# Performance work log

Hardware: AMD Instinct MI355X
Metric: run time of the kernel (lower is better)

Reference implementation:

```python
import jax, jax.numpy as jnp
import numpy as np
import math

B, S, H, DH = 8, 1024, 12, 64
HID = H * DH  # 768


def setup_inputs() -> dict:
    key = jax.random.key(0)
    ks = jax.random.split(key, 6)
    hidden_states = jax.random.normal(ks[0], (B, S, HID), dtype=jnp.float32)
    attention_mask = jax.random.bernoulli(ks[1], 0.1, (B, 1, 1, S))
    rel_pos = jax.random.normal(ks[2], (B, H, S, S), dtype=jnp.float32) * 0.1
    rel_2d_pos = jax.random.normal(ks[3], (B, H, S, S), dtype=jnp.float32) * 0.1
    W_qkv = jax.random.normal(ks[4], (HID, 3 * HID), dtype=jnp.float32) * (1.0 / math.sqrt(HID))
    q_bias = jnp.zeros((1, 1, HID), dtype=jnp.float32)
    v_bias = jnp.zeros((1, 1, HID), dtype=jnp.float32)
    return {
        "hidden_states": hidden_states,
        "attention_mask": attention_mask,
        "rel_pos": rel_pos,
        "rel_2d_pos": rel_2d_pos,
        "W_qkv": W_qkv,
        "q_bias": q_bias,
        "v_bias": v_bias,
    }


def reference(hidden_states, attention_mask, rel_pos, rel_2d_pos, W_qkv, q_bias, v_bias):
    b, s, _ = hidden_states.shape
    # fast_qkv: single GEMM, no bias; q/v get learned additive biases
    qkv = hidden_states @ W_qkv                       # [B,S,3*HID]
    q, k, v = jnp.split(qkv, 3, axis=-1)
    q = q + q_bias
    v = v + v_bias
    # [B,S,HID] -> [B,H,S,DH]
    def to_heads(x):
        return x.reshape(b, s, H, DH).transpose(0, 2, 1, 3)
    q, k, v = to_heads(q), to_heads(k), to_heads(v)
    q = q / math.sqrt(DH)
    scores = jnp.einsum('bhqd,bhkd->bhqk', q, k)      # [B,H,S,S]
    scores = scores + rel_pos + rel_2d_pos
    scores = jnp.where(attention_mask, -jnp.inf, scores.astype(jnp.float32))
    probs = jax.nn.softmax(scores, axis=-1).astype(v.dtype)
    context = jnp.einsum('bhqk,bhkd->bhqd', probs, v)  # [B,H,S,DH]
    context = context.transpose(0, 2, 1, 3).reshape(b, s, HID)
    return (context, probs)
```

## Files before the change

kernel.cpp:

```cpp
#include <hip/hip_runtime.h>
#include <hip/hip_bf16.h>

typedef __attribute__((ext_vector_type(8))) short short8;
typedef __attribute__((ext_vector_type(4))) float f32x4;

#define NB 8
#define NS 1024
#define NH 12
#define ND 64
#define NHID 768
#define N3 2304

#define SBAR() __builtin_amdgcn_sched_barrier(0)

__device__ __forceinline__ unsigned short f2bf(float f) {
  __hip_bfloat16 h = __float2bfloat16(f);
  return *reinterpret_cast<unsigned short*>(&h);
}
__device__ __forceinline__ float bf2f(unsigned short u) {
  __hip_bfloat16 h;
  *reinterpret_cast<unsigned short*>(&h) = u;
  return __bfloat162float(h);
}

__device__ __forceinline__ void gload_lds16(const unsigned short* g, unsigned short* l) {
  __builtin_amdgcn_global_load_lds(
      (const __attribute__((address_space(1))) unsigned int*)g,
      (__attribute__((address_space(3))) unsigned int*)l, 16, 0, 0);
}

__global__ void k_cast(const float* __restrict__ in, unsigned short* __restrict__ out, int n4) {
  int i = blockIdx.x * blockDim.x + threadIdx.x;
  if (i >= n4) return;
  float4 v = ((const float4*)in)[i];
  ushort4 o;
  o.x = f2bf(v.x); o.y = f2bf(v.y); o.z = f2bf(v.z); o.w = f2bf(v.w);
  ((ushort4*)out)[i] = o;
}

__global__ void k_mask(const int* __restrict__ mask, unsigned long long* __restrict__ bits) {
  int b = blockIdx.x, t = threadIdx.x;
  unsigned long long bal = __ballot(mask[b * NS + t] != 0);
  if ((t & 63) == 0) bits[b * 16 + (t >> 6)] = bal;
}

__global__ __launch_bounds__(256) void k_wt(const float* __restrict__ W, unsigned short* __restrict__ Wt) {
  __shared__ float tile[32][33];
  int r0 = blockIdx.x * 32;
  int c0 = blockIdx.y * 32;
  int tx = threadIdx.x & 31, ty = threadIdx.x >> 5;
#pragma unroll
  for (int p = 0; p < 4; ++p)
    tile[ty + 8*p][tx] = W[(size_t)(r0 + ty + 8*p) * N3 + c0 + tx];
  __syncthreads();
#pragma unroll
  for (int p = 0; p < 4; ++p)
    Wt[(size_t)(c0 + ty + 8*p) * NHID + r0 + tx] = f2bf(tile[tx][ty + 8*p]);
}

__global__ __launch_bounds__(256) void k_qkv(const unsigned short* __restrict__ A,
                                             const unsigned short* __restrict__ Wt,
                                             const float* __restrict__ qb,
                                             const float* __restrict__ vb,
                                             unsigned short* __restrict__ out) {
  __shared__ __align__(16) unsigned short As[128 * 32];
  __shared__ __align__(16) unsigned short Bs[128 * 32];
  const int t = threadIdx.x;
  const int w = t >> 6, l = t & 63, l15 = l & 15, lhi = l >> 4;
  const int wr = w >> 1, wc = w & 1;
  const int rowbase = blockIdx.x * 128;
  const int colbase = blockIdx.y * 128;
  const int srow = l >> 2;
  const int scol = (l & 3) * 8;

  f32x4 acc[4][4] = {};

  for (int k0 = 0; k0 < NHID; k0 += 32) {
    __syncthreads();
#pragma unroll
    for (int i = 0; i < 2; ++i) {
      int rr = w * 32 + i * 16;
      gload_lds16(A  + (size_t)(rowbase + rr + srow) * NHID + k0 + scol, As + rr * 32);
      gload_lds16(Wt + (size_t)(colbase + rr + srow) * NHID + k0 + scol, Bs + rr * 32);
    }
    __syncthreads();
    short8 a[4], bfr[4];
#pragma unroll
    for (int mi = 0; mi < 4; ++mi)
      a[mi] = *(const short8*)(As + (wr * 64 + mi * 16 + l15) * 32 + lhi * 8);
#pragma unroll
    for (int ni = 0; ni < 4; ++ni)
      bfr[ni] = *(const short8*)(Bs + (wc * 64 + ni * 16 + l15) * 32 + lhi * 8);
#pragma unroll
    for (int mi = 0; mi < 4; ++mi)
#pragma unroll
      for (int ni = 0; ni < 4; ++ni)
        acc[mi][ni] = __builtin_amdgcn_mfma_f32_16x16x32_bf16(a[mi], bfr[ni], acc[mi][ni], 0, 0, 0);
  }

  const int seg = colbase / NHID;
#pragma unroll
  for (int ni = 0; ni < 4; ++ni) {
    int col = colbase + wc * 64 + ni * 16 + l15;
    int cc = col % NHID;
    float bias = (seg == 0) ? qb[cc] : (seg == 2) ? vb[cc] : 0.0f;
#pragma unroll
    for (int mi = 0; mi < 4; ++mi)
#pragma unroll
      for (int r = 0; r < 4; ++r) {
        int row = rowbase + wr * 64 + mi * 16 + lhi * 4 + r;
        float v = acc[mi][ni][r];
        if (seg == 0) v = (v + bias) * 0.125f;
        else if (seg == 2) v = v + bias;
        out[(size_t)row * N3 + col] = f2bf(v);
      }
  }
}

__global__ __launch_bounds__(256) void k_vt(const unsigned short* __restrict__ qkvb,
                                            unsigned short* __restrict__ Vt) {
  __shared__ unsigned short tile[32][33];
  int s0 = blockIdx.x * 32;
  int d0 = blockIdx.y * 32;
  int bh = blockIdx.z;
  int b = bh / NH;
  int hcol = (bh % NH) * ND;
  int tx = threadIdx.x & 31, ty = threadIdx.x >> 5;
#pragma unroll
  for (int p = 0; p < 4; ++p) {
    int s = s0 + ty + 8*p;
    tile[ty + 8*p][tx] = qkvb[(size_t)(b * NS + s) * N3 + 2 * NHID + hcol + d0 + tx];
  }
  __syncthreads();
#pragma unroll
  for (int p = 0; p < 4; ++p) {
    int d = d0 + ty + 8*p;
    Vt[((size_t)bh * ND + d) * NS + s0 + tx] = tile[tx][ty + 8*p];
  }
}

__global__ __launch_bounds__(256, 2) void k_attn(const unsigned short* __restrict__ qkvb,
                                                 const unsigned short* __restrict__ Vt,
                                                 const float* __restrict__ relp,
                                                 const float* __restrict__ rel2,
                                                 const unsigned long long* __restrict__ mbits,
                                                 float* __restrict__ outp) {
  __shared__ __align__(16) char Ks[2][16384];
  __shared__ __align__(16) char Vs[2][16384];
  __shared__ __align__(16) char Rs[2][4096];
  __shared__ __align__(16) unsigned short stg[4][16][40];
  __shared__ float rs_lds[4][16];
  __shared__ float inv_lds[16];

  const int qt = blockIdx.x, h = blockIdx.y, b = blockIdx.z;
  const int t = threadIdx.x, w = t >> 6, l = t & 63, l15 = l & 15, lhi = l >> 4;
  const int bh = b * NH + h;

  const int skk = t >> 1;
  const int skc = (t & 1) * 64;
  const int svd = t >> 2;
  const int svc = (t & 3) * 64;
  const int srr = t >> 4;
  const int src = (t & 15) * 8;
  const int kwz = (skk & 7) << 4, vwz = (svd & 7) << 4, rwz = (srr & 7) << 4;
  const int rotw = (skk >> 3) & 3;
  const int rotv = ((svd >> 3) & 1) + 2 * ((svc >> 7) & 1);

  const unsigned short* qrowp = qkvb + (size_t)(b * NS + qt * 16 + l15) * N3 + h * ND;
  short8 qa0 = *(const short8*)(qrowp + lhi * 8);
  short8 qa1 = *(const short8*)(qrowp + 32 + lhi * 8);

  unsigned long long mw[8];
#pragma unroll
  for (int c = 0; c < 8; ++c) mw[c] = mbits[b * 16 + c * 2 + (w >> 1)];

  const unsigned short* kgbase = qkvb + (size_t)(b * NS + skk) * N3 + NHID + h * ND + (skc >> 1);
  const unsigned short* vgbase = Vt + (size_t)(bh * ND + svd) * NS + (svc >> 1);
  const float* rgbase  = relp + ((size_t)(bh * NS + qt * 16 + srr)) * NS + src;
  const float* r2gbase = rel2 + ((size_t)(bh * NS + qt * 16 + srr)) * NS + src;

  short8 kr0, kr1, kr2, kr3, vr0, vr1, vr2, vr3;
  float4 relA[3][2], rel2A[3][2];

#define KV_LOAD(c) do {                                                 \
    const unsigned short* kg = kgbase + (size_t)(c) * 128 * N3;         \
    kr0 = *(const short8*)(kg);      kr1 = *(const short8*)(kg + 8);    \
    kr2 = *(const short8*)(kg + 16); kr3 = *(const short8*)(kg + 24);   \
    const unsigned short* vg = vgbase + (c) * 128;                      \
    vr0 = *(const short8*)(vg);      vr1 = *(const short8*)(vg + 8);    \
    vr2 = *(const short8*)(vg + 16); vr3 = *(const short8*)(vg + 24);   \
  } while (0)

#define R_LOAD(c, sl) do {                                              \
    const float* rg = rgbase + (c) * 128;                               \
    relA[sl][0]  = *(const float4*)(rg);                                \
    relA[sl][1]  = *(const float4*)(rg + 4);                            \
    const float* r2g = r2gbase + (c) * 128;                             \
    rel2A[sl][0] = *(const float4*)(r2g);                               \
    rel2A[sl][1] = *(const float4*)(r2g + 4);                           \
  } while (0)

#define KV_WRITE(buf) do {                                                        \
    char* KB = Ks[buf];                                                           \
    *(short8*)(KB + skk * 128 + ((skc + 16 * ((0 + rotw) & 3)) ^ kwz)) = kr0;     \
    *(short8*)(KB + skk * 128 + ((skc + 16 * ((1 + rotw) & 3)) ^ kwz)) = kr1;     \
    *(short8*)(KB + skk * 128 + ((skc + 16 * ((2 + rotw) & 3)) ^ kwz)) = kr2;     \
    *(short8*)(KB + skk * 128 + ((skc + 16 * ((3 + rotw) & 3)) ^ kwz)) = kr3;     \
    char* VB = Vs[buf];                                                           \
    *(short8*)(VB + svd * 256 + ((svc + 16 * ((0 + rotv) & 3)) ^ vwz)) = vr0;     \
    *(short8*)(VB + svd * 256 + ((svc + 16 * ((1 + rotv) & 3)) ^ vwz)) = vr1;     \
    *(short8*)(VB + svd * 256 + ((svc + 16 * ((2 + rotv) & 3)) ^ vwz)) = vr2;     \
    *(short8*)(VB + svd * 256 + ((svc + 16 * ((3 + rotv) & 3)) ^ vwz)) = vr3;     \
  } while (0)

#define R_WRITE(buf, sl) do {                                                     \
    char* RB = Rs[buf];                                                           \
    ushort4 u0, u1;                                                               \
    u0.x = f2bf(relA[sl][0].x + rel2A[sl][0].x);                                  \
    u0.y = f2bf(relA[sl][0].y + rel2A[sl][0].y);                                  \
    u0.z = f2bf(relA[sl][0].z + rel2A[sl][0].z);                                  \
    u0.w = f2bf(relA[sl][0].w + rel2A[sl][0].w);                                  \
    u1.x = f2bf(relA[sl][1].x + rel2A[sl][1].x);                                  \
    u1.y = f2bf(relA[sl][1].y + rel2A[sl][1].y);                                  \
    u1.z = f2bf(relA[sl][1].z + rel2A[sl][1].z);                                  \
    u1.w = f2bf(relA[sl][1].w + rel2A[sl][1].w);                                  \
    *(ushort4*)(RB + srr * 256 + ((src * 2 + 0) ^ rwz)) = u0;                     \
    *(ushort4*)(RB + srr * 256 + ((src * 2 + 8) ^ rwz)) = u1;                     \
  } while (0)

  unsigned int pkA[8][2], pkB[8][2];
  f32x4 cacc[4] = {};
  float rs = 0.f;

  R_LOAD(0, 0); R_LOAD(1, 1); R_LOAD(2, 2);
  KV_LOAD(0);
#pragma unroll
  for (int c = 0; c < 8; ++c) {
    const int buf = c & 1;
    KV_WRITE(buf);
    R_WRITE(buf, c % 3);
    SBAR();
    if (c < 7) KV_LOAD(c + 1);
    if (c < 5) R_LOAD(c + 3, c % 3);
    SBAR();
    __syncthreads();

    const char* KB = Ks[buf]; const char* VB = Vs[buf]; const char* RB = Rs[buf];
#pragma unroll
    for (int s = 0; s < 2; ++s) {
      int kkr = w * 32 + s * 16 + l15;
      int kx = (kkr & 7) << 4;
      int rotr = (kkr >> 3) & 3;
      short8 kf0 = *(const short8*)(KB + kkr * 128 + ((16 * ((lhi + rotr) & 3)) ^ kx));
      short8 kf1 = *(const short8*)(KB + kkr * 128 + ((64 + 16 * ((lhi + rotr) & 3)) ^ kx));
      f32x4 sc = {};
      sc = __builtin_amdgcn_mfma_f32_16x16x32_bf16(kf0, qa0, sc, 0, 0, 0);
      sc = __builtin_amdgcn_mfma_f32_16x16x32_bf16(kf1, qa1, sc, 0, 0, 0);
      ushort4 rsu = *(const ushort4*)(RB + l15 * 256 + ((w * 64 + s * 32 + lhi * 8) ^ ((l15 & 7) << 4)));
      int mb = (int)((mw[c] >> ((w & 1) * 32 + s * 16 + lhi * 4)) & 0xFull);
      float p0 = (mb & 1) ? 0.f : __expf(sc[0] + bf2f(rsu.x));
      float p1 = (mb & 2) ? 0.f : __expf(sc[1] + bf2f(rsu.y));
      float p2 = (mb & 4) ? 0.f : __expf(sc[2] + bf2f(rsu.z));
      float p3 = (mb & 8) ? 0.f : __expf(sc[3] + bf2f(rsu.w));
      rs += (p0 + p1) + (p2 + p3);
      ushort4 pw;
      pw.x = f2bf(p0); pw.y = f2bf(p1); pw.z = f2bf(p2); pw.w = f2bf(p3);
      pkA[c][s] = (unsigned int)pw.x | ((unsigned int)pw.y << 16);
      pkB[c][s] = (unsigned int)pw.z | ((unsigned int)pw.w << 16);
      *(ushort4*)(&stg[w][l15][s * 16 + lhi * 4]) = pw;
    }
    SBAR();
    short8 pa = *(const short8*)(&stg[w][l15][lhi * 8]);
#pragma unroll
    for (int n = 0; n < 4; ++n) {
      int dr = n * 16 + l15;
      int rotvr = ((dr >> 3) & 1) + 2 * ((w >> 1) & 1);
      short8 vf = *(const short8*)(VB + dr * 256 + ((w * 64 + 16 * ((lhi + rotvr) & 3)) ^ ((dr & 7) << 4)));
      cacc[n] = __builtin_amdgcn_mfma_f32_16x16x32_bf16(pa, vf, cacc[n], 0, 0, 0);
    }
  }

  rs += __shfl_xor(rs, 16);
  rs += __shfl_xor(rs, 32);
  if (lhi == 0) rs_lds[w][l15] = rs;
  __syncthreads();
  if (t < 16)
    inv_lds[t] = 1.0f / (rs_lds[0][t] + rs_lds[1][t] + rs_lds[2][t] + rs_lds[3][t]);

  {
    char* PB = (char*)Vs;
    int psw = (l15 & 7) << 4;
#pragma unroll
    for (int c = 0; c < 8; ++c)
#pragma unroll
      for (int s = 0; s < 2; ++s) {
        int colb = (c * 128 + w * 32 + s * 16 + lhi * 4) * 2;
        uint2 u; u.x = pkA[c][s]; u.y = pkB[c][s];
        *(uint2*)(PB + l15 * 2048 + (colb ^ psw)) = u;
      }
  }
  {
    float* cpart = (float*)Ks;
#pragma unroll
    for (int n = 0; n < 4; ++n)
#pragma unroll
      for (int r = 0; r < 4; ++r)
        cpart[w * 1024 + (lhi * 4 + r) * 64 + n * 16 + l15] = cacc[n][r];
  }
  __syncthreads();

  {
    float* probs = outp + (size_t)NB * NS * NHID;
    const char* PB = (const char*)Vs;
#pragma unroll
    for (int rr = 0; rr < 4; ++rr) {
      int row = w * 4 + rr;
      float inv = inv_lds[row];
      int sz = (row & 7) << 4;
      size_t base = ((size_t)bh * NS + qt * 16 + row) * NS;
#pragma unroll
      for (int i = 0; i < 4; ++i) {
        int cols = 4 * l + 256 * i;
        ushort4 pv = *(const ushort4*)(PB + row * 2048 + ((cols * 2) ^ sz));
        float4 o;
        o.x = bf2f(pv.x) * inv;
        o.y = bf2f(pv.y) * inv;
        o.z = bf2f(pv.z) * inv;
        o.w = bf2f(pv.w) * inv;
        *(float4*)(&probs[base + cols]) = o;
      }
    }
  }

  {
    const float* cpart = (const float*)Ks;
#pragma unroll
    for (int i = 0; i < 4; ++i) {
      int idx = t + 256 * i;
      int q = idx >> 6, d = idx & 63;
      float s = cpart[idx] + cpart[1024 + idx] + cpart[2048 + idx] + cpart[3072 + idx];
      outp[(size_t)(b * NS + qt * 16 + q) * NHID + h * ND + d] = s * inv_lds[q];
    }
  }
#undef KV_LOAD
#undef R_LOAD
#undef KV_WRITE
#undef R_WRITE
}

extern "C" void kernel_launch(void* const* d_in, const int* in_sizes, int n_in,
                              void* d_out, int out_size, void* d_ws, size_t ws_size,
                              hipStream_t stream) {
  const float* hidden = (const float*)d_in[0];
  const int* mask = (const int*)d_in[1];
  const float* relp = (const float*)d_in[2];
  const float* rel2 = (const float*)d_in[3];
  const float* Wq = (const float*)d_in[4];
  const float* qb = (const float*)d_in[5];
  const float* vb = (const float*)d_in[6];
  float* out = (float*)d_out;

  const size_t OFF_AHS = 0;
  const size_t OFF_WT  = 12582912;
  const size_t OFF_QKV = 16121856;
  const size_t OFF_VT  = 53870592;
  const size_t OFF_MB  = 66453504;
  if (ws_size < 66454528) return;

  char* ws = (char*)d_ws;
  unsigned short* Ahs  = (unsigned short*)(ws + OFF_AHS);
  unsigned short* Wt   = (unsigned short*)(ws + OFF_WT);
  unsigned short* qkvb = (unsigned short*)(ws + OFF_QKV);
  unsigned short* Vt   = (unsigned short*)(ws + OFF_VT);
  unsigned long long* mb = (unsigned long long*)(ws + OFF_MB);

  k_cast<<<dim3(6144), dim3(256), 0, stream>>>(hidden, Ahs, (NB * NS * NHID) / 4);
  k_mask<<<dim3(8), dim3(1024), 0, stream>>>(mask, mb);
  k_wt<<<dim3(24, 72), dim3(256), 0, stream>>>(Wq, Wt);
  k_qkv<<<dim3(64, 18), dim3(256), 0, stream>>>(Ahs, Wt, qb, vb, qkvb);
  k_vt<<<dim3(32, 2, 96), dim3(256), 0, stream>>>(qkvb, Vt);
  k_attn<<<dim3(64, 12, 8), dim3(256), 0, stream>>>(qkvb, Vt, relp, rel2, mb, out);
}
```

Baseline: 347.9 us.

## Drop V LDS staging, load V fragments directly from global to raise occupancy

Removes the 32KB V shared-memory double buffer and has each wave load its V^T MFMA fragments straight from global memory each chunk. The mask words are now loaded once per chunk instead of held in registers, and the context reduction is split into two halves through the small Rs buffer. Together these cut LDS and register use, and launch bounds rise to 3 blocks per CU. In exchange, V loads are exposed and not prefetched, and the epilogue gains extra barriers.

Result: slower. 417.1 us (+19.9%).

```diff
diff --git a/kernel.cpp b/kernel.cpp
--- a/kernel.cpp
+++ b/kernel.cpp
@@ -139,14 +139,13 @@
   }
 }
 
-__global__ __launch_bounds__(256, 2) void k_attn(const unsigned short* __restrict__ qkvb,
+__global__ __launch_bounds__(256, 3) void k_attn(const unsigned short* __restrict__ qkvb,
                                                  const unsigned short* __restrict__ Vt,
                                                  const float* __restrict__ relp,
                                                  const float* __restrict__ rel2,
                                                  const unsigned long long* __restrict__ mbits,
                                                  float* __restrict__ outp) {
   __shared__ __align__(16) char Ks[2][16384];
-  __shared__ __align__(16) char Vs[2][16384];
   __shared__ __align__(16) char Rs[2][4096];
   __shared__ __align__(16) unsigned short stg[4][16][40];
   __shared__ float rs_lds[4][16];
@@ -158,37 +157,27 @@
 
   const int skk = t >> 1;
   const int skc = (t & 1) * 64;
-  const int svd = t >> 2;
-  const int svc = (t & 3) * 64;
   const int srr = t >> 4;
   const int src = (t & 15) * 8;
-  const int kwz = (skk & 7) << 4, vwz = (svd & 7) << 4, rwz = (srr & 7) << 4;
+  const int kwz = (skk & 7) << 4, rwz = (srr & 7) << 4;
   const int rotw = (skk >> 3) & 3;
-  const int rotv = ((svd >> 3) & 1) + 2 * ((svc >> 7) & 1);
 
   const unsigned short* qrowp = qkvb + (size_t)(b * NS + qt * 16 + l15) * N3 + h * ND;
   short8 qa0 = *(const short8*)(qrowp + lhi * 8);
   short8 qa1 = *(const short8*)(qrowp + 32 + lhi * 8);
 
-  unsigned long long mw[8];
-#pragma unroll
-  for (int c = 0; c < 8; ++c) mw[c] = mbits[b * 16 + c * 2 + (w >> 1)];
-
   const unsigned short* kgbase = qkvb + (size_t)(b * NS + skk) * N3 + NHID + h * ND + (skc >> 1);
-  const unsigned short* vgbase = Vt + (size_t)(bh * ND + svd) * NS + (svc >> 1);
+  const unsigned short* vtb = Vt + (size_t)bh * ND * NS;
   const float* rgbase  = relp + ((size_t)(bh * NS + qt * 16 + srr)) * NS + src;
   const float* r2gbase = rel2 + ((size_t)(bh * NS + qt * 16 + srr)) * NS + src;
 
-  short8 kr0, kr1, kr2, kr3, vr0, vr1, vr2, vr3;
+  short8 kr0, kr1, kr2, kr3;
   float4 relA[3][2], rel2A[3][2];
 
-#define KV_LOAD(c) do {                                                 \
+#define K_LOAD(c) do {                                                  \
     const unsigned short* kg = kgbase + (size_t)(c) * 128 * N3;         \
     kr0 = *(const short8*)(kg);      kr1 = *(const short8*)(kg + 8);    \
     kr2 = *(const short8*)(kg + 16); kr3 = *(const short8*)(kg + 24);   \
-    const unsigned short* vg = vgbase + (c) * 128;                      \
-    vr0 = *(const short8*)(vg);      vr1 = *(const short8*)(vg + 8);    \
-    vr2 = *(const short8*)(vg + 16); vr3 = *(const short8*)(vg + 24);   \
   } while (0)
 
 #define R_LOAD(c, sl) do {                                              \
@@ -200,17 +189,12 @@
     rel2A[sl][1] = *(const float4*)(r2g + 4);                           \
   } while (0)
 
-#define KV_WRITE(buf) do {                                                        \
+#define K_WRITE(buf) do {                                                         \
     char* KB = Ks[buf];                                                           \
     *(short8*)(KB + skk * 128 + ((skc + 16 * ((0 + rotw) & 3)) ^ kwz)) = kr0;     \
     *(short8*)(KB + skk * 128 + ((skc + 16 * ((1 + rotw) & 3)) ^ kwz)) = kr1;     \
     *(short8*)(KB + skk * 128 + ((skc + 16 * ((2 + rotw) & 3)) ^ kwz)) = kr2;     \
     *(short8*)(KB + skk * 128 + ((skc + 16 * ((3 + rotw) & 3)) ^ kwz)) = kr3;     \
-    char* VB = Vs[buf];                                                           \
-    *(short8*)(VB + svd * 256 + ((svc + 16 * ((0 + rotv) & 3)) ^ vwz)) = vr0;     \
-    *(short8*)(VB + svd * 256 + ((svc + 16 * ((1 + rotv) & 3)) ^ vwz)) = vr1;     \
-    *(short8*)(VB + svd * 256 + ((svc + 16 * ((2 + rotv) & 3)) ^ vwz)) = vr2;     \
-    *(short8*)(VB + svd * 256 + ((svc + 16 * ((3 + rotv) & 3)) ^ vwz)) = vr3;     \
   } while (0)
 
 #define R_WRITE(buf, sl) do {                                                     \
@@ -232,20 +216,26 @@
   f32x4 cacc[4] = {};
   float rs = 0.f;
 
+  K_LOAD(0);
   R_LOAD(0, 0); R_LOAD(1, 1); R_LOAD(2, 2);
-  KV_LOAD(0);
 #pragma unroll
   for (int c = 0; c < 8; ++c) {
     const int buf = c & 1;
-    KV_WRITE(buf);
+    K_WRITE(buf);
     R_WRITE(buf, c % 3);
     SBAR();
-    if (c < 7) KV_LOAD(c + 1);
+    if (c < 7) K_LOAD(c + 1);
     if (c < 5) R_LOAD(c + 3, c % 3);
     SBAR();
     __syncthreads();
 
-    const char* KB = Ks[buf]; const char* VB = Vs[buf]; const char* RB = Rs[buf];
+    short8 vf0 = *(const short8*)(vtb + (size_t)(0 * 16 + l15) * NS + c * 128 + w * 32 + lhi * 8);
+    short8 vf1 = *(const short8*)(vtb + (size_t)(1 * 16 + l15) * NS + c * 128 + w * 32 + lhi * 8);
+    short8 vf2 = *(const short8*)(vtb + (size_t)(2 * 16 + l15) * NS + c * 128 + w * 32 + lhi * 8);
+    short8 vf3 = *(const short8*)(vtb + (size_t)(3 * 16 + l15) * NS + c * 128 + w * 32 + lhi * 8);
+
+    const char* KB = Ks[buf]; const char* RB = Rs[buf];
+    unsigned long long mwc = mbits[b * 16 + c * 2 + (w >> 1)];
 #pragma unroll
     for (int s = 0; s < 2; ++s) {
       int kkr = w * 32 + s * 16 + l15;
@@ -257,7 +247,7 @@
       sc = __builtin_amdgcn_mfma_f32_16x16x32_bf16(kf0, qa0, sc, 0, 0, 0);
       sc = __builtin_amdgcn_mfma_f32_16x16x32_bf16(kf1, qa1, sc, 0, 0, 0);
       ushort4 rsu = *(const ushort4*)(RB + l15 * 256 + ((w * 64 + s * 32 + lhi * 8) ^ ((l15 & 7) << 4)));
-      int mb = (int)((mw[c] >> ((w & 1) * 32 + s * 16 + lhi * 4)) & 0xFull);
+      int mb = (int)((mwc >> ((w & 1) * 32 + s * 16 + lhi * 4)) & 0xFull);
       float p0 = (mb & 1) ? 0.f : __expf(sc[0] + bf2f(rsu.x));
       float p1 = (mb & 2) ? 0.f : __expf(sc[1] + bf2f(rsu.y));
       float p2 = (mb & 4) ? 0.f : __expf(sc[2] + bf2f(rsu.z));
@@ -271,13 +261,10 @@
     }
     SBAR();
     short8 pa = *(const short8*)(&stg[w][l15][lhi * 8]);
-#pragma unroll
-    for (int n = 0; n < 4; ++n) {
-      int dr = n * 16 + l15;
-      int rotvr = ((dr >> 3) & 1) + 2 * ((w >> 1) & 1);
-      short8 vf = *(const short8*)(VB + dr * 256 + ((w * 64 + 16 * ((lhi + rotvr) & 3)) ^ ((dr & 7) << 4)));
-      cacc[n] = __builtin_amdgcn_mfma_f32_16x16x32_bf16(pa, vf, cacc[n], 0, 0, 0);
-    }
+    cacc[0] = __builtin_amdgcn_mfma_f32_16x16x32_bf16(pa, vf0, cacc[0], 0, 0, 0);
+    cacc[1] = __builtin_amdgcn_mfma_f32_16x16x32_bf16(pa, vf1, cacc[1], 0, 0, 0);
+    cacc[2] = __builtin_amdgcn_mfma_f32_16x16x32_bf16(pa, vf2, cacc[2], 0, 0, 0);
+    cacc[3] = __builtin_amdgcn_mfma_f32_16x16x32_bf16(pa, vf3, cacc[3], 0, 0, 0);
   }
 
   rs += __shfl_xor(rs, 16);
@@ -288,7 +275,7 @@
     inv_lds[t] = 1.0f / (rs_lds[0][t] + rs_lds[1][t] + rs_lds[2][t] + rs_lds[3][t]);
 
   {
-    char* PB = (char*)Vs;
+    char* PB = (char*)Ks;
     int psw = (l15 & 7) << 4;
 #pragma unroll
     for (int c = 0; c < 8; ++c)
@@ -300,18 +287,29 @@
       }
   }
   {
-    float* cpart = (float*)Ks;
-#pragma unroll
-    for (int n = 0; n < 4; ++n)
+    float* cp = (float*)Rs;
+#pragma unroll
+    for (int n = 0; n < 2; ++n)
 #pragma unroll
       for (int r = 0; r < 4; ++r)
-        cpart[w * 1024 + (lhi * 4 + r) * 64 + n * 16 + l15] = cacc[n][r];
-  }
-  __syncthreads();
+        cp[w * 512 + (lhi * 4 + r) * 32 + n * 16 + l15] = cacc[n][r];
+  }
+  __syncthreads();
+
+  {
+    const float* cp = (const float*)Rs;
+#pragma unroll
+    for (int i = 0; i < 2; ++i) {
+      int idx = t + 256 * i;
+      int q = idx >> 5, d = idx & 31;
+      float s = cp[q * 32 + d] + cp[512 + q * 32 + d] + cp[1024 + q * 32 + d] + cp[1536 + q * 32 + d];
+      outp[(size_t)(b * NS + qt * 16 + q) * NHID + h * ND + d] = s * inv_lds[q];
+    }
+  }
 
   {
     float* probs = outp + (size_t)NB * NS * NHID;
-    const char* PB = (const char*)Vs;
+    const char* PB = (const char*)Ks;
 #pragma unroll
     for (int rr = 0; rr < 4; ++rr) {
       int row = w * 4 + rr;
@@ -332,19 +330,29 @@
     }
   }
 
-  {
-    const float* cpart = (const float*)Ks;
-#pragma unroll
-    for (int i = 0; i < 4; ++i) {
+  __syncthreads();
+  {
+    float* cp = (float*)Rs;
+#pragma unroll
+    for (int n = 2; n < 4; ++n)
+#pragma unroll
+      for (int r = 0; r < 4; ++r)
+        cp[w * 512 + (lhi * 4 + r) * 32 + (n - 2) * 16 + l15] = cacc[n][r];
+  }
+  __syncthreads();
+  {
+    const float* cp = (const float*)Rs;
+#pragma unroll
+    for (int i = 0; i < 2; ++i) {
       int idx = t + 256 * i;
-      int q = idx >> 6, d = idx & 63;
-      float s = cpart[idx] + cpart[1024 + idx] + cpart[2048 + idx] + cpart[3072 + idx];
-      outp[(size_t)(b * NS + qt * 16 + q) * NHID + h * ND + d] = s * inv_lds[q];
-    }
-  }
-#undef KV_LOAD
+      int q = idx >> 5, d = idx & 31;
+      float s = cp[q * 32 + d] + cp[512 + q * 32 + d] + cp[1024 + q * 32 + d] + cp[1536 + q * 32 + d];
+      outp[(size_t)(b * NS + qt * 16 + q) * NHID + h * ND + 32 + d] = s * inv_lds[q];
+    }
+  }
+#undef K_LOAD
 #undef R_LOAD
-#undef KV_WRITE
+#undef K_WRITE
 #undef R_WRITE
 }
 
```
